# Kernel tuning notes

Hardware: AMD Instinct MI355X
Metric: run time of the kernel (lower is better)

Reference implementation:

```python
import jax, jax.numpy as jnp
import numpy as np

N, OBS_LEN, PRED_LEN = 8192, 20, 30
EMBED, HIDDEN, CNN_OUT = 64, 128, 2048


def setup_inputs() -> dict:
    key = jax.random.key(0)
    ks = jax.random.split(key, 13)
    s = 0.05
    return {
        "img_embedding": jax.random.normal(ks[0], (N, CNN_OUT), jnp.float32),
        "obs_pos": jax.random.normal(ks[1], (N, OBS_LEN, 2), jnp.float32),
        "obs_hist_size": jax.random.randint(ks[2], (N,), 0, 20, jnp.int64) if jax.config.jax_enable_x64 else jax.random.randint(ks[2], (N,), 0, 20, jnp.int32),
        "obs_pos_rel": jax.random.normal(ks[3], (N, OBS_LEN, 2), jnp.float32),
        "h0": jax.random.normal(ks[4], (1, HIDDEN), jnp.float32) * s,
        "W_ih": jax.random.normal(ks[5], (4 * HIDDEN, EMBED), jnp.float32) * s,
        "W_hh": jax.random.normal(ks[6], (4 * HIDDEN, HIDDEN), jnp.float32) * s,
        "b_ih": jax.random.normal(ks[7], (4 * HIDDEN,), jnp.float32) * s,
        "b_hh": jax.random.normal(ks[8], (4 * HIDDEN,), jnp.float32) * s,
        "embed_W": jax.random.normal(ks[9], (EMBED, 2), jnp.float32) * s,
        "embed_b": jax.random.normal(ks[10], (EMBED,), jnp.float32) * s,
        "pred_W": jax.random.normal(ks[11], (2, HIDDEN + CNN_OUT), jnp.float32) * s,
        "pred_b": jax.random.normal(ks[12], (2,), jnp.float32) * s,
    }


def reference(img_embedding, obs_pos, obs_hist_size, obs_pos_rel,
              h0, W_ih, W_hh, b_ih, b_hh, embed_W, embed_b, pred_W, pred_b):
    n, obs_len = obs_pos.shape[0], obs_pos.shape[1]

    def lstm_cell(x_emb, h, c):
        # torch gate order: i, f, g, o
        gates = x_emb @ W_ih.T + b_ih + h @ W_hh.T + b_hh  # [n, 4H]
        i, f, g, o = jnp.split(gates, 4, axis=-1)
        c2 = jax.nn.sigmoid(f) * c + jax.nn.sigmoid(i) * jnp.tanh(g)
        h2 = jax.nn.sigmoid(o) * jnp.tanh(c2)
        return h2, c2

    def embed(rel):
        return jax.nn.relu(rel @ embed_W.T + embed_b)

    # NOTE: original code initializes BOTH h and c from h0 (faithful to source).
    h = jnp.broadcast_to(h0, (n, h0.shape[1]))
    c = h

    # ---- observation phase: t = 1 .. obs_len-1, masked update ----
    def obs_step(carry, inp):
        h, c = carry
        rel_t, t = inp
        mask = (obs_hist_size > (obs_len - t))[:, None]  # [n, 1]
        h2, c2 = lstm_cell(embed(rel_t), h, c)
        h = jnp.where(mask, h2, h)
        c = jnp.where(mask, c2, c)
        return (h, c), None

    ts = jnp.arange(1, obs_len)
    rel_seq = jnp.swapaxes(obs_pos_rel[:, 1:, :], 0, 1)  # [obs_len-1, n, 2]
    (h, c), _ = jax.lax.scan(obs_step, (h, c), (rel_seq, ts))

    def pred_step(carry, _):
        h, c, pos = carry
        disp = jnp.concatenate([h, img_embedding], axis=1) @ pred_W.T + pred_b  # [n, 2]
        pos = pos + disp
        h, c = lstm_cell(embed(disp), h, c)
        return (h, c, pos), pos

    pos0 = obs_pos[:, -1, :]
    _, traj = jax.lax.scan(pred_step, (h, c, pos0), None, length=PRED_LEN)
    return jnp.swapaxes(traj, 0, 1)  # [n, pred_len, 2]
```

## Files before the change

kernel.cpp:

```cpp
#include <hip/hip_runtime.h>

#define MBLK 32

typedef __attribute__((ext_vector_type(8))) short bf16x8;
typedef __attribute__((ext_vector_type(16))) float f32x16;

__device__ __forceinline__ unsigned short f2bf(float x){
  unsigned int u = __float_as_uint(x);
  u = u + 0x7FFFu + ((u >> 16) & 1u);
  return (unsigned short)(u >> 16);
}
__device__ __forceinline__ float bf2f(unsigned short s){
  return __uint_as_float(((unsigned int)s) << 16);
}
__device__ __forceinline__ float sigm(float x){
  return __builtin_amdgcn_rcpf(1.0f + __expf(-x));
}
__device__ __forceinline__ float tanh_(float x){
  return 1.0f - 2.0f*__builtin_amdgcn_rcpf(__expf(2.0f*x) + 1.0f);
}
__device__ __forceinline__ unsigned int pk_bf16(float lo, float hi){
  unsigned int r;
  asm("v_cvt_pk_bf16_f32 %0, %1, %2" : "=v"(r) : "v"(lo), "v"(hi));
  return r;
}

__global__ __launch_bounds__(512, 2) void traj_kernel(
    const float* __restrict__ img, const float* __restrict__ obs_pos,
    const int* __restrict__ hist, const float* __restrict__ rel,
    const float* __restrict__ h0, const float* __restrict__ W_ih,
    const float* __restrict__ W_hh, const float* __restrict__ b_ih,
    const float* __restrict__ b_hh, const float* __restrict__ eW,
    const float* __restrict__ eb, const float* __restrict__ pW,
    const float* __restrict__ pb, float* __restrict__ out)
{
  __shared__ unsigned short xh[2][MBLK*200];
  __shared__ float relL[MBLK*40];
  __shared__ float pwL[256];
  __shared__ float imgcL[MBLK*2];

  const int tid   = threadIdx.x;
  const int wv    = tid >> 6;
  const int lane  = tid & 63;
  const int m     = lane & 31;
  const int khalf = lane >> 5;
  const int hb    = khalf*4;
  const int g0    = blockIdx.x * MBLK;
  const int dm    = tid >> 4;
  const int i16   = tid & 15;

  for (int idx = tid; idx < MBLK*40; idx += 512) relL[idx] = rel[g0*40 + idx];
  if (tid < 256) pwL[tid] = pW[(tid >> 7)*2176 + (tid & 127)];

  {
    const float* row = img + (size_t)(g0 + dm)*2048 + i16*128;
    const float* p0  = pW + 128 + i16*128;
    const float* p1  = pW + 2176 + 128 + i16*128;
    float s0 = 0.f, s1 = 0.f;
    #pragma unroll
    for (int v = 0; v < 32; v++){
      float4 a  = ((const float4*)row)[v];
      float4 w0 = ((const float4*)p0)[v];
      float4 w1 = ((const float4*)p1)[v];
      s0 += a.x*w0.x + a.y*w0.y + a.z*w0.z + a.w*w0.w;
      s1 += a.x*w1.x + a.y*w1.y + a.z*w1.z + a.w*w1.w;
    }
    #pragma unroll
    for (int msk = 1; msk < 16; msk <<= 1){
      s0 += __shfl_xor(s0, msk);
      s1 += __shfl_xor(s1, msk);
    }
    if (i16 == 0){ imgcL[dm*2] = s0; imgcL[dm*2+1] = s1; }
  }

  const int   e0  = i16*4;
  const float wA0 = eW[e0*2],       wB0 = eW[e0*2+1];
  const float wA1 = eW[(e0+1)*2],   wB1 = eW[(e0+1)*2+1];
  const float wA2 = eW[(e0+2)*2],   wB2 = eW[(e0+2)*2+1];
  const float wA3 = eW[(e0+3)*2],   wB3 = eW[(e0+3)*2+1];
  const float be0 = eb[e0], be1 = eb[e0+1], be2 = eb[e0+2], be3 = eb[e0+3];
  const float pb0r = pb[0], pb1r = pb[1];

  const int thr = 20 - hist[g0 + m];
  float c_s[8];
  #pragma unroll
  for (int t = 0; t < 8; t++) c_s[t] = h0[wv*16 + hb + (t&3) + 8*(t>>2)];

  {
    int mm = tid >> 4, j8 = (tid & 15)*8;
    #pragma unroll
    for (int e = 0; e < 8; e++)
      xh[0][mm*200 + 64 + j8 + e] = f2bf(h0[j8 + e]);
  }

  bf16x8 Bf[2][13];
  #pragma unroll
  for (int T = 0; T < 2; T++){
    int nrow = (T*2 + (m >> 4))*128 + wv*16 + (m & 15);
    #pragma unroll
    for (int ks = 0; ks < 12; ks++){
      const float* src = (ks < 4) ? (W_ih + nrow*64  + ks*16     + khalf*8)
                                  : (W_hh + nrow*128 + (ks-4)*16 + khalf*8);
      float4 lo = ((const float4*)src)[0];
      float4 hi = ((const float4*)src)[1];
      bf16x8 tf;
      tf[0]=(short)f2bf(lo.x); tf[1]=(short)f2bf(lo.y); tf[2]=(short)f2bf(lo.z); tf[3]=(short)f2bf(lo.w);
      tf[4]=(short)f2bf(hi.x); tf[5]=(short)f2bf(hi.y); tf[6]=(short)f2bf(hi.z); tf[7]=(short)f2bf(hi.w);
      Bf[T][ks] = tf;
    }
    bf16x8 bb;
    #pragma unroll
    for (int e = 0; e < 8; e++) bb[e] = 0;
    if (khalf == 0) bb[0] = (short)f2bf(b_ih[nrow] + b_hh[nrow]);
    Bf[T][12] = bb;
  }
  bf16x8 Bone;
  #pragma unroll
  for (int e = 0; e < 8; e++) Bone[e] = 0;
  if (khalf == 0) Bone[0] = (short)0x3F80;

  float pos_r = 0.f;
  if (i16 < 2) pos_r = obs_pos[(size_t)(g0 + dm)*40 + 38 + i16];

  __syncthreads();

  const float imgc0 = imgcL[dm*2], imgc1 = imgcL[dm*2+1];

  {
    float2 rr = *((const float2*)&relL[dm*40 + 2]);
    float a0 = fmaxf(0.f, rr.x*wA0 + rr.y*wB0 + be0);
    float a1 = fmaxf(0.f, rr.x*wA1 + rr.y*wB1 + be1);
    float a2 = fmaxf(0.f, rr.x*wA2 + rr.y*wB2 + be2);
    float a3 = fmaxf(0.f, rr.x*wA3 + rr.y*wB3 + be3);
    *((uint2*)&xh[0][dm*200 + e0]) = make_uint2(pk_bf16(a0,a1), pk_bf16(a2,a3));
  }

  const int hofs = m*200 + 64 + wv*16 + hb;
  int b = 0;

  for (int step = 0; step < 49; step++){
    const bool obs = (step < 19);
    __syncthreads();

    f32x16 a0, a1;
    #pragma unroll
    for (int e = 0; e < 16; e++){ a0[e] = 0.f; a1[e] = 0.f; }

    if (obs){
      a0 = __builtin_amdgcn_mfma_f32_32x32x16_bf16(Bf[0][12], Bone, a0, 0, 0, 0);
      a1 = __builtin_amdgcn_mfma_f32_32x32x16_bf16(Bf[1][12], Bone, a1, 0, 0, 0);
      {
        bf16x8 X[6];
        #pragma unroll
        for (int ks = 0; ks < 6; ks++)
          X[ks] = *((const bf16x8*)&xh[b][m*200 + ks*16 + khalf*8]);
        #pragma unroll
        for (int ks = 0; ks < 6; ks++){
          a0 = __builtin_amdgcn_mfma_f32_32x32x16_bf16(Bf[0][ks], X[ks], a0, 0, 0, 0);
          a1 = __builtin_amdgcn_mfma_f32_32x32x16_bf16(Bf[1][ks], X[ks], a1, 0, 0, 0);
        }
      }
      {
        bf16x8 X[6];
        #pragma unroll
        for (int ks = 0; ks < 6; ks++)
          X[ks] = *((const bf16x8*)&xh[b][m*200 + (6+ks)*16 + khalf*8]);
        #pragma unroll
        for (int ks = 0; ks < 6; ks++){
          a0 = __builtin_amdgcn_mfma_f32_32x32x16_bf16(Bf[0][6+ks], X[ks], a0, 0, 0, 0);
          a1 = __builtin_amdgcn_mfma_f32_32x32x16_bf16(Bf[1][6+ks], X[ks], a1, 0, 0, 0);
        }
      }
      if (step < 18){
        int tt = step + 2;
        float2 rr = *((const float2*)&relL[dm*40 + tt*2]);
        float x0 = fmaxf(0.f, rr.x*wA0 + rr.y*wB0 + be0);
        float x1 = fmaxf(0.f, rr.x*wA1 + rr.y*wB1 + be1);
        float x2 = fmaxf(0.f, rr.x*wA2 + rr.y*wB2 + be2);
        float x3 = fmaxf(0.f, rr.x*wA3 + rr.y*wB3 + be3);
        *((uint2*)&xh[b^1][dm*200 + e0]) = make_uint2(pk_bf16(x0,x1), pk_bf16(x2,x3));
      }
    } else {
      bf16x8 Xh[8];
      #pragma unroll
      for (int ks = 0; ks < 8; ks++)
        Xh[ks] = *((const bf16x8*)&xh[b][m*200 + 64 + ks*16 + khalf*8]);

      bf16x8 hv = *((const bf16x8*)&xh[b][dm*200 + 64 + i16*8]);
      float4 pa0 = *((const float4*)&pwL[i16*8]);
      float4 pa1 = *((const float4*)&pwL[i16*8 + 4]);
      float4 pc0 = *((const float4*)&pwL[128 + i16*8]);
      float4 pc1 = *((const float4*)&pwL[128 + i16*8 + 4]);
      float s0, s1;
      {
        float h0f = bf2f((unsigned short)hv[0]), h1f = bf2f((unsigned short)hv[1]);
        float h2f = bf2f((unsigned short)hv[2]), h3f = bf2f((unsigned short)hv[3]);
        float h4f = bf2f((unsigned short)hv[4]), h5f = bf2f((unsigned short)hv[5]);
        float h6f = bf2f((unsigned short)hv[6]), h7f = bf2f((unsigned short)hv[7]);
        s0 = h0f*pa0.x + h1f*pa0.y + h2f*pa0.z + h3f*pa0.w
           + h4f*pa1.x + h5f*pa1.y + h6f*pa1.z + h7f*pa1.w;
        s1 = h0f*pc0.x + h1f*pc0.y + h2f*pc0.z + h3f*pc0.w
           + h4f*pc1.x + h5f*pc1.y + h6f*pc1.z + h7f*pc1.w;
      }

      a0 = __builtin_amdgcn_mfma_f32_32x32x16_bf16(Bf[0][12], Bone, a0, 0, 0, 0);
      a1 = __builtin_amdgcn_mfma_f32_32x32x16_bf16(Bf[1][12], Bone, a1, 0, 0, 0);
      #pragma unroll
      for (int ks = 0; ks < 8; ks++){
        a0 = __builtin_amdgcn_mfma_f32_32x32x16_bf16(Bf[0][4+ks], Xh[ks], a0, 0, 0, 0);
        a1 = __builtin_amdgcn_mfma_f32_32x32x16_bf16(Bf[1][4+ks], Xh[ks], a1, 0, 0, 0);
      }

      s0 += __shfl_xor(s0, 1);  s1 += __shfl_xor(s1, 1);
      s0 += __shfl_xor(s0, 2);  s1 += __shfl_xor(s1, 2);
      s0 += __shfl_xor(s0, 4);  s1 += __shfl_xor(s1, 4);
      s0 += __shfl_xor(s0, 8);  s1 += __shfl_xor(s1, 8);
      float d0 = s0 + imgc0 + pb0r;
      float d1 = s1 + imgc1 + pb1r;
      if (i16 < 2){
        pos_r += (i16 == 0) ? d0 : d1;
        out[(size_t)(g0 + dm)*60 + (size_t)(step - 19)*2 + i16] = pos_r;
      }
      float x0 = fmaxf(0.f, d0*wA0 + d1*wB0 + be0);
      float x1 = fmaxf(0.f, d0*wA1 + d1*wB1 + be1);
      float x2 = fmaxf(0.f, d0*wA2 + d1*wB2 + be2);
      float x3 = fmaxf(0.f, d0*wA3 + d1*wB3 + be3);
      *((uint2*)&xh[b][dm*200 + e0]) = make_uint2(pk_bf16(x0,x1), pk_bf16(x2,x3));

      __syncthreads();
      #pragma unroll
      for (int ks = 0; ks < 4; ks++){
        bf16x8 Xx = *((const bf16x8*)&xh[b][m*200 + ks*16 + khalf*8]);
        a0 = __builtin_amdgcn_mfma_f32_32x32x16_bf16(Bf[0][ks], Xx, a0, 0, 0, 0);
        a1 = __builtin_amdgcn_mfma_f32_32x32x16_bf16(Bf[1][ks], Xx, a1, 0, 0, 0);
      }
    }

    float h2f[8];
    #pragma unroll
    for (int t = 0; t < 8; t++){
      float ig = a0[t];
      float fg = a0[8+t];
      float gg = a1[t];
      float og = a1[8+t];
      float c2 = sigm(fg)*c_s[t] + sigm(ig)*tanh_(gg);
      float h2 = sigm(og)*tanh_(c2);
      if (obs && (step < thr)) c2 = c_s[t];
      c_s[t] = c2;
      h2f[t] = h2;
    }

    uint2 Qa = make_uint2(pk_bf16(h2f[0], h2f[1]), pk_bf16(h2f[2], h2f[3]));
    uint2 Qb = make_uint2(pk_bf16(h2f[4], h2f[5]), pk_bf16(h2f[6], h2f[7]));
    if (obs && (step < thr)){
      Qa = *((const uint2*)&xh[b][hofs]);
      Qb = *((const uint2*)&xh[b][hofs + 8]);
    }
    *((uint2*)&xh[b^1][hofs])     = Qa;
    *((uint2*)&xh[b^1][hofs + 8]) = Qb;

    b ^= 1;
  }
}

extern "C" void kernel_launch(void* const* d_in, const int* in_sizes, int n_in,
                              void* d_out, int out_size, void* d_ws, size_t ws_size,
                              hipStream_t stream){
  const float* img     = (const float*)d_in[0];
  const float* obs_pos = (const float*)d_in[1];
  const int*   hist    = (const int*)d_in[2];
  const float* rel     = (const float*)d_in[3];
  const float* h0      = (const float*)d_in[4];
  const float* W_ih    = (const float*)d_in[5];
  const float* W_hh    = (const float*)d_in[6];
  const float* b_ih    = (const float*)d_in[7];
  const float* b_hh    = (const float*)d_in[8];
  const float* eW      = (const float*)d_in[9];
  const float* eb      = (const float*)d_in[10];
  const float* pW      = (const float*)d_in[11];
  const float* pb      = (const float*)d_in[12];
  float* out = (float*)d_out;
  hipLaunchKernelGGL(traj_kernel, dim3(8192/MBLK), dim3(512), 0, stream,
                     img, obs_pos, hist, rel, h0, W_ih, W_hh, b_ih, b_hh,
                     eW, eb, pW, pb, out);
}
```

Baseline: 255.2 us.

## Precompute hidden-state projection partials in LSTM epilogue and fold bias into accumulator init

```diff
diff --git a/kernel.cpp b/kernel.cpp
--- a/kernel.cpp
+++ b/kernel.cpp
@@ -36,8 +36,8 @@
 {
   __shared__ unsigned short xh[2][MBLK*200];
   __shared__ float relL[MBLK*40];
-  __shared__ float pwL[256];
   __shared__ float imgcL[MBLK*2];
+  __shared__ float2 pdL[32][17];
 
   const int tid   = threadIdx.x;
   const int wv    = tid >> 6;
@@ -50,7 +50,6 @@
   const int i16   = tid & 15;
 
   for (int idx = tid; idx < MBLK*40; idx += 512) relL[idx] = rel[g0*40 + idx];
-  if (tid < 256) pwL[tid] = pW[(tid >> 7)*2176 + (tid & 127)];
 
   {
     const float* row = img + (size_t)(g0 + dm)*2048 + i16*128;
@@ -81,6 +80,14 @@
   const float be0 = eb[e0], be1 = eb[e0+1], be2 = eb[e0+2], be3 = eb[e0+3];
   const float pb0r = pb[0], pb1r = pb[1];
 
+  float pwa[8], pwb[8];
+  #pragma unroll
+  for (int t = 0; t < 8; t++){
+    int ht = wv*16 + hb + (t&3) + 8*(t>>2);
+    pwa[t] = pW[ht];
+    pwb[t] = pW[2176 + ht];
+  }
+
   const int thr = 20 - hist[g0 + m];
   float c_s[8];
   #pragma unroll
@@ -93,7 +100,7 @@
       xh[0][mm*200 + 64 + j8 + e] = f2bf(h0[j8 + e]);
   }
 
-  bf16x8 Bf[2][13];
+  bf16x8 Bf[2][12];
   #pragma unroll
   for (int T = 0; T < 2; T++){
     int nrow = (T*2 + (m >> 4))*128 + wv*16 + (m & 15);
@@ -108,16 +115,26 @@
       tf[4]=(short)f2bf(hi.x); tf[5]=(short)f2bf(hi.y); tf[6]=(short)f2bf(hi.z); tf[7]=(short)f2bf(hi.w);
       Bf[T][ks] = tf;
     }
-    bf16x8 bb;
-    #pragma unroll
-    for (int e = 0; e < 8; e++) bb[e] = 0;
-    if (khalf == 0) bb[0] = (short)f2bf(b_ih[nrow] + b_hh[nrow]);
-    Bf[T][12] = bb;
-  }
-  bf16x8 Bone;
-  #pragma unroll
-  for (int e = 0; e < 8; e++) Bone[e] = 0;
-  if (khalf == 0) Bone[0] = (short)0x3F80;
+  }
+
+  f32x16 bias0, bias1;
+  {
+    f32x16 z;
+    #pragma unroll
+    for (int e = 0; e < 16; e++) z[e] = 0.f;
+    bf16x8 one, bb0, bb1;
+    #pragma unroll
+    for (int e = 0; e < 8; e++){ one[e] = 0; bb0[e] = 0; bb1[e] = 0; }
+    if (khalf == 0){
+      one[0] = (short)0x3F80;
+      int nr0 = ((m >> 4))*128 + wv*16 + (m & 15);
+      int nr1 = (2 + (m >> 4))*128 + wv*16 + (m & 15);
+      bb0[0] = (short)f2bf(b_ih[nr0] + b_hh[nr0]);
+      bb1[0] = (short)f2bf(b_ih[nr1] + b_hh[nr1]);
+    }
+    bias0 = __builtin_amdgcn_mfma_f32_32x32x16_bf16(bb0, one, z, 0, 0, 0);
+    bias1 = __builtin_amdgcn_mfma_f32_32x32x16_bf16(bb1, one, z, 0, 0, 0);
+  }
 
   float pos_r = 0.f;
   if (i16 < 2) pos_r = obs_pos[(size_t)(g0 + dm)*40 + 38 + i16];
@@ -136,26 +153,27 @@
   }
 
   const int hofs = m*200 + 64 + wv*16 + hb;
+  const unsigned short* xb0 = &xh[0][m*200 + khalf*8];
+  const unsigned short* xb1 = &xh[1][m*200 + khalf*8];
   int b = 0;
 
   for (int step = 0; step < 49; step++){
     const bool obs = (step < 19);
     __syncthreads();
 
+    const unsigned short* xr = b ? xb1 : xb0;
     f32x16 a0, a1;
-    #pragma unroll
-    for (int e = 0; e < 16; e++){ a0[e] = 0.f; a1[e] = 0.f; }
 
     if (obs){
-      a0 = __builtin_amdgcn_mfma_f32_32x32x16_bf16(Bf[0][12], Bone, a0, 0, 0, 0);
-      a1 = __builtin_amdgcn_mfma_f32_32x32x16_bf16(Bf[1][12], Bone, a1, 0, 0, 0);
       {
         bf16x8 X[6];
         #pragma unroll
         for (int ks = 0; ks < 6; ks++)
-          X[ks] = *((const bf16x8*)&xh[b][m*200 + ks*16 + khalf*8]);
+          X[ks] = *((const bf16x8*)&xr[ks*16]);
+        a0 = __builtin_amdgcn_mfma_f32_32x32x16_bf16(Bf[0][0], X[0], bias0, 0, 0, 0);
+        a1 = __builtin_amdgcn_mfma_f32_32x32x16_bf16(Bf[1][0], X[0], bias1, 0, 0, 0);
         #pragma unroll
-        for (int ks = 0; ks < 6; ks++){
+        for (int ks = 1; ks < 6; ks++){
           a0 = __builtin_amdgcn_mfma_f32_32x32x16_bf16(Bf[0][ks], X[ks], a0, 0, 0, 0);
           a1 = __builtin_amdgcn_mfma_f32_32x32x16_bf16(Bf[1][ks], X[ks], a1, 0, 0, 0);
         }
@@ -164,7 +182,7 @@
         bf16x8 X[6];
         #pragma unroll
         for (int ks = 0; ks < 6; ks++)
-          X[ks] = *((const bf16x8*)&xh[b][m*200 + (6+ks)*16 + khalf*8]);
+          X[ks] = *((const bf16x8*)&xr[(6+ks)*16]);
         #pragma unroll
         for (int ks = 0; ks < 6; ks++){
           a0 = __builtin_amdgcn_mfma_f32_32x32x16_bf16(Bf[0][6+ks], X[ks], a0, 0, 0, 0);
@@ -184,29 +202,15 @@
       bf16x8 Xh[8];
       #pragma unroll
       for (int ks = 0; ks < 8; ks++)
-        Xh[ks] = *((const bf16x8*)&xh[b][m*200 + 64 + ks*16 + khalf*8]);
-
-      bf16x8 hv = *((const bf16x8*)&xh[b][dm*200 + 64 + i16*8]);
-      float4 pa0 = *((const float4*)&pwL[i16*8]);
-      float4 pa1 = *((const float4*)&pwL[i16*8 + 4]);
-      float4 pc0 = *((const float4*)&pwL[128 + i16*8]);
-      float4 pc1 = *((const float4*)&pwL[128 + i16*8 + 4]);
-      float s0, s1;
-      {
-        float h0f = bf2f((unsigned short)hv[0]), h1f = bf2f((unsigned short)hv[1]);
-        float h2f = bf2f((unsigned short)hv[2]), h3f = bf2f((unsigned short)hv[3]);
-        float h4f = bf2f((unsigned short)hv[4]), h5f = bf2f((unsigned short)hv[5]);
-        float h6f = bf2f((unsigned short)hv[6]), h7f = bf2f((unsigned short)hv[7]);
-        s0 = h0f*pa0.x + h1f*pa0.y + h2f*pa0.z + h3f*pa0.w
-           + h4f*pa1.x + h5f*pa1.y + h6f*pa1.z + h7f*pa1.w;
-        s1 = h0f*pc0.x + h1f*pc0.y + h2f*pc0.z + h3f*pc0.w
-           + h4f*pc1.x + h5f*pc1.y + h6f*pc1.z + h7f*pc1.w;
-      }
-
-      a0 = __builtin_amdgcn_mfma_f32_32x32x16_bf16(Bf[0][12], Bone, a0, 0, 0, 0);
-      a1 = __builtin_amdgcn_mfma_f32_32x32x16_bf16(Bf[1][12], Bone, a1, 0, 0, 0);
+        Xh[ks] = *((const bf16x8*)&xr[(4+ks)*16]);
+
+      float2 pp = pdL[dm][i16];
+      float s0 = pp.x, s1 = pp.y;
+
+      a0 = __builtin_amdgcn_mfma_f32_32x32x16_bf16(Bf[0][4], Xh[0], bias0, 0, 0, 0);
+      a1 = __builtin_amdgcn_mfma_f32_32x32x16_bf16(Bf[1][4], Xh[0], bias1, 0, 0, 0);
       #pragma unroll
-      for (int ks = 0; ks < 8; ks++){
+      for (int ks = 1; ks < 8; ks++){
         a0 = __builtin_amdgcn_mfma_f32_32x32x16_bf16(Bf[0][4+ks], Xh[ks], a0, 0, 0, 0);
         a1 = __builtin_amdgcn_mfma_f32_32x32x16_bf16(Bf[1][4+ks], Xh[ks], a1, 0, 0, 0);
       }
@@ -230,7 +234,7 @@
       __syncthreads();
       #pragma unroll
       for (int ks = 0; ks < 4; ks++){
-        bf16x8 Xx = *((const bf16x8*)&xh[b][m*200 + ks*16 + khalf*8]);
+        bf16x8 Xx = *((const bf16x8*)&xr[ks*16]);
         a0 = __builtin_amdgcn_mfma_f32_32x32x16_bf16(Bf[0][ks], Xx, a0, 0, 0, 0);
         a1 = __builtin_amdgcn_mfma_f32_32x32x16_bf16(Bf[1][ks], Xx, a1, 0, 0, 0);
       }
@@ -258,6 +262,22 @@
     }
     *((uint2*)&xh[b^1][hofs])     = Qa;
     *((uint2*)&xh[b^1][hofs + 8]) = Qb;
+
+    if (step >= 18 && step < 48){
+      float v0 = bf2f((unsigned short)(Qa.x & 0xFFFFu));
+      float v1 = bf2f((unsigned short)(Qa.x >> 16));
+      float v2 = bf2f((unsigned short)(Qa.y & 0xFFFFu));
+      float v3 = bf2f((unsigned short)(Qa.y >> 16));
+      float v4 = bf2f((unsigned short)(Qb.x & 0xFFFFu));
+      float v5 = bf2f((unsigned short)(Qb.x >> 16));
+      float v6 = bf2f((unsigned short)(Qb.y & 0xFFFFu));
+      float v7 = bf2f((unsigned short)(Qb.y >> 16));
+      float pd0 = v0*pwa[0] + v1*pwa[1] + v2*pwa[2] + v3*pwa[3]
+                + v4*pwa[4] + v5*pwa[5] + v6*pwa[6] + v7*pwa[7];
+      float pd1 = v0*pwb[0] + v1*pwb[1] + v2*pwb[2] + v3*pwb[3]
+                + v4*pwb[4] + v5*pwb[5] + v6*pwb[6] + v7*pwb[7];
+      pdL[m][wv*2 + khalf] = make_float2(pd0, pd1);
+    }
 
     b ^= 1;
   }
```

Result: slower. 267.6 us (+4.8%).
